# Performance work log

Measured on AMD Instinct MI355X. Metric: run time of the kernel, lower is better.

The kernel has to match this reference:

```python
import jax, jax.numpy as jnp
import numpy as np

B, S, D = 32, 4096, 512  # batch, src seq len, hidden (n_hidden_in == n_hidden_out)


def setup_inputs() -> dict:
    key = jax.random.key(0)
    k1, k2, k3, k4 = jax.random.split(key, 4)
    return {
        "hidden_targ": jax.random.normal(k1, (B, D), dtype=jnp.float32),
        "hidden_src": jax.random.normal(k2, (B, S, D), dtype=jnp.float32),
        "mask": jnp.ones((B, S), dtype=jnp.float32),
        "W": jax.random.normal(k3, (D, 2 * D), dtype=jnp.float32) * (2 * D) ** -0.5,
        "V": jax.random.uniform(k4, (D,), dtype=jnp.float32),
    }


def reference(hidden_targ, hidden_src, mask, W, V):
    # W @ cat(targ, src) == targ @ Wt^T + src @ Ws^T  (avoids materializing the
    # repeated/concatenated [b, s, 2d] tensor the torch code builds)
    d = hidden_targ.shape[-1]
    Wt, Ws = W[:, :d], W[:, d:]
    # [b, 1, h] + [b, s, h] -> tanh pre-activation
    pre = jnp.tanh(
        jnp.einsum("bd,hd->bh", hidden_targ, Wt)[:, None, :]
        + jnp.einsum("bsd,hd->bsh", hidden_src, Ws)
    )
    e = jnp.einsum("bsh,h->bs", pre, V)            # scores [b, s]
    att_weights = jax.nn.softmax(e, axis=1) * mask  # softmax then mask (as in source)
    ctx = jnp.einsum("bs,bsd->bd", att_weights, hidden_src)
    hidden_output = ctx + hidden_targ
    return att_weights, hidden_output
```

## Files before the change

### kernel.cpp

```cpp
#include <hip/hip_runtime.h>
#include <hip/hip_bf16.h>


typedef __attribute__((ext_vector_type(8))) short bf16x8;
typedef __attribute__((ext_vector_type(4))) float f32x4;

#define BM 128
#define BN 128
#define BKK 32
#define LDA 40

static __device__ __forceinline__ unsigned pack2(float a, float b) {
    unsigned ua = __float_as_uint(a), ub = __float_as_uint(b);
    unsigned ra = (ua + 0x7fffu + ((ua >> 16) & 1u)) >> 16;
    unsigned rb = (ub + 0x7fffu + ((ub >> 16) & 1u)) & 0xffff0000u;
    return ra | rb;
}

static __device__ __forceinline__ void async_load16(const void* g, void* l) {
    __builtin_amdgcn_global_load_lds(
        (const __attribute__((address_space(1))) void*)g,
        (__attribute__((address_space(3))) void*)l, 16, 0, 0);
}

static __device__ __forceinline__ float fast_tanh(float x) {
    float ex = exp2f(x * 2.8853900817779268f);
    return 1.0f - 2.0f / (ex + 1.0f);
}

__global__ void wconv_kernel(const float* __restrict__ W, short* __restrict__ wbf) {
    const int gid = blockIdx.x * 256 + threadIdx.x;
    const int tile = gid >> 9, p = gid & 511;
    const int hx = tile >> 4, ktile = tile & 15;
    const int r = p >> 2, up = p & 3;
    const int u = up ^ ((r >> 1) & 3);
    const float* s = W + (long)(hx * 128 + r) * 1024 + 512 + ktile * 32 + u * 8;
    float4 v0 = *(const float4*)(s);
    float4 v1 = *(const float4*)(s + 4);
    uint4 pk;
    pk.x = pack2(v0.x, v0.y); pk.y = pack2(v0.z, v0.w);
    pk.z = pack2(v1.x, v1.y); pk.w = pack2(v1.z, v1.w);
    ((uint4*)wbf)[gid] = pk;
}

__global__ void t_kernel(const float* __restrict__ targ,
                         const float* __restrict__ W,
                         float* __restrict__ t) {
    __shared__ float tg[512];
    const int b = blockIdx.x >> 2;
    const int hbase = (blockIdx.x & 3) * 128;
    const int tid = threadIdx.x;
    tg[tid]       = targ[b * 512 + tid];
    tg[tid + 256] = targ[b * 512 + tid + 256];
    __syncthreads();
    const int lane = tid & 63, wave = tid >> 6;
    for (int h = hbase + wave; h < hbase + 128; h += 4) {
        const float* wr = W + (long)h * 1024;
        float s = 0.f;
        #pragma unroll
        for (int i = 0; i < 2; i++) {
            const int d = lane * 4 + i * 256;
            float4 wv = *(const float4*)(wr + d);
            s += wv.x * tg[d] + wv.y * tg[d + 1] + wv.z * tg[d + 2] + wv.w * tg[d + 3];
        }
        s += __shfl_xor(s, 1);  s += __shfl_xor(s, 2);  s += __shfl_xor(s, 4);
        s += __shfl_xor(s, 8);  s += __shfl_xor(s, 16); s += __shfl_xor(s, 32);
        if (lane == 0) t[b * 512 + h] = s;
    }
}

__global__ __launch_bounds__(256, 2)
void gemm_e_kernel(const float* __restrict__ src,
                   const short* __restrict__ wbf,
                   const float* __restrict__ t,
                   const float* __restrict__ V,
                   float* __restrict__ e) {
    __shared__ __align__(16) short As[BM * LDA];
    __shared__ __align__(16) short Bs[BN * BKK];

    const int tid = threadIdx.x;
    const int L = blockIdx.x;
    const int mt = (L >> 5) * 8 + (L & 7);
    const int hx = (L >> 3) & 3;
    const long m0 = (long)mt * BM;
    const int b = (int)(m0 >> 12);

    const int lane = tid & 63;
    const int wave = tid >> 6;
    const int wm = wave & 1, wn = wave >> 1;
    const int lr = lane & 15, quad = lane >> 4;

    f32x4 acc[4][4];
    #pragma unroll
    for (int i = 0; i < 4; i++)
        #pragma unroll
        for (int j = 0; j < 4; j++)
            acc[i][j] = (f32x4){0.f, 0.f, 0.f, 0.f};

    const int arow = tid >> 1, ah = (tid & 1) * 16;

    for (int kt = 0; kt < 512; kt += BKK) {
        __syncthreads();
        const short* chunk = wbf + (long)(hx * 16 + (kt >> 5)) * 4096;
        async_load16(chunk + tid * 8, Bs + tid * 8);
        async_load16(chunk + 2048 + tid * 8, Bs + 2048 + tid * 8);
        const float* ap = src + (m0 + arow) * 512 + kt + ah;
        float4 v0 = *(const float4*)(ap);
        float4 v1 = *(const float4*)(ap + 4);
        float4 v2 = *(const float4*)(ap + 8);
        float4 v3 = *(const float4*)(ap + 12);
        uint4 pA, pB;
        pA.x = pack2(v0.x, v0.y); pA.y = pack2(v0.z, v0.w);
        pA.z = pack2(v1.x, v1.y); pA.w = pack2(v1.z, v1.w);
        pB.x = pack2(v2.x, v2.y); pB.y = pack2(v2.z, v2.w);
        pB.z = pack2(v3.x, v3.y); pB.w = pack2(v3.z, v3.w);
        *(uint4*)(As + arow * LDA + ah)     = pA;
        *(uint4*)(As + arow * LDA + ah + 8) = pB;
        __syncthreads();

        bf16x8 af[4], bfr[4];
        #pragma unroll
        for (int mi = 0; mi < 4; mi++)
            af[mi] = *(const bf16x8*)(As + (wm * 64 + mi * 16 + lr) * LDA + quad * 8);
        #pragma unroll
        for (int ni = 0; ni < 4; ni++) {
            const int row = wn * 64 + ni * 16 + lr;
            const int q = quad ^ ((row >> 1) & 3);
            bfr[ni] = *(const bf16x8*)(Bs + row * 32 + q * 8);
        }
        #pragma unroll
        for (int mi = 0; mi < 4; mi++)
            #pragma unroll
            for (int ni = 0; ni < 4; ni++)
                acc[mi][ni] = __builtin_amdgcn_mfma_f32_16x16x32_bf16(
                    af[mi], bfr[ni], acc[mi][ni], 0, 0, 0);
    }

    const float* trow = t + b * 512;
    float th[4], vv[4];
    #pragma unroll
    for (int ni = 0; ni < 4; ni++) {
        const int h = hx * 128 + wn * 64 + ni * 16 + lr;
        th[ni] = trow[h];
        vv[ni] = V[h];
    }
    #pragma unroll
    for (int mi = 0; mi < 4; mi++) {
        #pragma unroll
        for (int r = 0; r < 4; r++) {
            float es = 0.f;
            #pragma unroll
            for (int ni = 0; ni < 4; ni++) {
                float val = acc[mi][ni][r] + th[ni];
                es += fast_tanh(val) * vv[ni];
            }
            es += __shfl_xor(es, 1);
            es += __shfl_xor(es, 2);
            es += __shfl_xor(es, 4);
            es += __shfl_xor(es, 8);
            if (lr == 0) {
                const long m = m0 + wm * 64 + mi * 16 + quad * 4 + r;
                atomicAdd(&e[m], es);
            }
        }
    }
}

__global__ void stats_kernel(const float* __restrict__ e, float* __restrict__ stats) {
    const int b = blockIdx.x, tid = threadIdx.x;
    __shared__ float red[256];
    float mx = -1e30f;
    for (int s = tid; s < 4096; s += 256) mx = fmaxf(mx, e[b * 4096 + s]);
    red[tid] = mx; __syncthreads();
    for (int st = 128; st > 0; st >>= 1) {
        if (tid < st) red[tid] = fmaxf(red[tid], red[tid + st]);
        __syncthreads();
    }
    mx = red[0]; __syncthreads();
    float sm = 0.f;
    for (int s = tid; s < 4096; s += 256)
        sm += exp2f((e[b * 4096 + s] - mx) * 1.4426950408889634f);
    red[tid] = sm; __syncthreads();
    for (int st = 128; st > 0; st >>= 1) {
        if (tid < st) red[tid] += red[tid + st];
        __syncthreads();
    }
    if (tid == 0) { stats[b * 2] = mx; stats[b * 2 + 1] = red[0]; }
}

__global__ __launch_bounds__(256)
void ctx_kernel(const float* __restrict__ e, const float* __restrict__ stats,
                const float* __restrict__ mask, const float* __restrict__ src,
                float* __restrict__ att, float* __restrict__ outh) {
    const int b = blockIdx.y;
    const int s0 = blockIdx.x * 256;
    const int tid = threadIdx.x;
    __shared__ float ash[256];
    __shared__ float4 part[128];

    const float mx = stats[b * 2];
    const float inv = 1.0f / stats[b * 2 + 1];
    const int s = s0 + tid;
    float a = exp2f((e[b * 4096 + s] - mx) * 1.4426950408889634f) * inv
              * mask[b * 4096 + s];
    att[(long)b * 4096 + s] = a;
    ash[tid] = a;
    __syncthreads();

    const int half = tid >> 7, d4 = tid & 127;
    float4 acc = {0.f, 0.f, 0.f, 0.f};
    const float4* s4 = (const float4*)(src + ((long)b * 4096 + s0) * 512);
    #pragma unroll 4
    for (int i = half; i < 256; i += 2) {
        float4 v = s4[(long)i * 128 + d4];
        float w = ash[i];
        acc.x += w * v.x; acc.y += w * v.y; acc.z += w * v.z; acc.w += w * v.w;
    }
    if (half) part[d4] = acc;
    __syncthreads();
    if (!half) {
        float4 p = part[d4];
        acc.x += p.x; acc.y += p.y; acc.z += p.z; acc.w += p.w;
        float* o = outh + b * 512 + d4 * 4;
        atomicAdd(o + 0, acc.x); atomicAdd(o + 1, acc.y);
        atomicAdd(o + 2, acc.z); atomicAdd(o + 3, acc.w);
    }
}

extern "C" void kernel_launch(void* const* d_in, const int* in_sizes, int n_in,
                              void* d_out, int out_size, void* d_ws, size_t ws_size,
                              hipStream_t stream) {
    const float* targ = (const float*)d_in[0];
    const float* src  = (const float*)d_in[1];
    const float* mask = (const float*)d_in[2];
    const float* W    = (const float*)d_in[3];
    const float* V    = (const float*)d_in[4];

    float* att  = (float*)d_out;
    float* outh = (float*)d_out + 131072;

    float* e  = (float*)d_ws;
    float* t  = e + 131072;
    float* st = t + 16384;
    short* wbf = (short*)((char*)d_ws + 590080);

    hipMemsetAsync(e, 0, 131072 * sizeof(float), stream);
    hipMemcpyAsync(outh, targ, 16384 * sizeof(float), hipMemcpyDeviceToDevice, stream);

    wconv_kernel<<<128, 256, 0, stream>>>(W, wbf);
    t_kernel<<<128, 256, 0, stream>>>(targ, W, t);
    gemm_e_kernel<<<4096, 256, 0, stream>>>(src, wbf, t, V, e);
    stats_kernel<<<32, 256, 0, stream>>>(e, st);
    ctx_kernel<<<dim3(16, 32), 256, 0, stream>>>(e, st, mask, src, att, outh);
}
```

Before: 503.8 us.

## Pre-convert src to swizzled bf16 and replace atomics with partial-sum buffers

When the workspace is large enough, a new kernel converts the whole src tensor once into a swizzled bf16 tile layout. The GEMM then streams it straight into LDS with async loads, and the context reduction reads the bf16 copy instead of fp32. This targets two costs: each src tile being converted to bf16 separately in all four h-blocks that reuse it, and the fp32 re-read in the ctx pass. Atomic accumulation of scores and context is replaced by per-block partial buffers, which a stats kernel and a new final kernel reduce, so the memset and copy launches go away. The trade-offs are an extra full pass writing 128MB of bf16, lower precision in the context sum, and reliance on a large workspace, with an fp32 fallback path otherwise.

Measured after the change: 553.2 us. +9.8%, slower.

```diff
diff --git a/kernel.cpp b/kernel.cpp
--- a/kernel.cpp
+++ b/kernel.cpp
@@ -6,7 +6,6 @@
 typedef __attribute__((ext_vector_type(4))) float f32x4;
 
 #define BM 128
-#define BN 128
 #define BKK 32
 #define LDA 40
 
@@ -17,6 +16,10 @@
     return ra | rb;
 }
 
+static __device__ __forceinline__ float bf2f(short s) {
+    return __uint_as_float(((unsigned)(unsigned short)s) << 16);
+}
+
 static __device__ __forceinline__ void async_load16(const void* g, void* l) {
     __builtin_amdgcn_global_load_lds(
         (const __attribute__((address_space(1))) void*)g,
@@ -27,6 +30,15 @@
     float ex = exp2f(x * 2.8853900817779268f);
     return 1.0f - 2.0f / (ex + 1.0f);
 }
+
+#define WS_WBF     0L
+#define WS_EPART   524288L
+#define WS_E       2621440L
+#define WS_T       3145728L
+#define WS_STATS   3211264L
+#define WS_CTXP    3211520L
+#define WS_SRCBF   4260096L
+#define WS_NEED_A  (WS_SRCBF + 134217728L)
 
 __global__ void wconv_kernel(const float* __restrict__ W, short* __restrict__ wbf) {
     const int gid = blockIdx.x * 256 + threadIdx.x;
@@ -43,6 +55,22 @@
     ((uint4*)wbf)[gid] = pk;
 }
 
+__global__ void srcconv_kernel(const float* __restrict__ src, short* __restrict__ sbf) {
+    const long gid = (long)blockIdx.x * 256 + threadIdx.x;
+    const long tile = gid >> 9;
+    const int p = (int)(gid & 511);
+    const long mt = tile >> 4; const int kt = (int)(tile & 15);
+    const int r = p >> 2, up = p & 3;
+    const int u = up ^ ((r >> 1) & 3);
+    const float* s = src + (mt * 128 + r) * 512 + kt * 32 + u * 8;
+    float4 v0 = *(const float4*)(s);
+    float4 v1 = *(const float4*)(s + 4);
+    uint4 pk;
+    pk.x = pack2(v0.x, v0.y); pk.y = pack2(v0.z, v0.w);
+    pk.z = pack2(v1.x, v1.y); pk.w = pack2(v1.z, v1.w);
+    ((uint4*)sbf)[gid] = pk;
+}
+
 __global__ void t_kernel(const float* __restrict__ targ,
                          const float* __restrict__ W,
                          float* __restrict__ t) {
@@ -69,14 +97,106 @@
     }
 }
 
-__global__ __launch_bounds__(256, 2)
-void gemm_e_kernel(const float* __restrict__ src,
+__global__ __launch_bounds__(256, 4)
+void gemm_a_kernel(const short* __restrict__ sbf,
                    const short* __restrict__ wbf,
                    const float* __restrict__ t,
                    const float* __restrict__ V,
-                   float* __restrict__ e) {
+                   float* __restrict__ epart) {
+    __shared__ __align__(16) short As[4096];
+    __shared__ __align__(16) short Bs[4096];
+    __shared__ float er[2][128];
+
+    const int tid = threadIdx.x;
+    const int L = blockIdx.x;
+    const int mt = (L >> 5) * 8 + (L & 7);
+    const int hx = (L >> 3) & 3;
+    const long m0 = (long)mt * BM;
+    const int b = (int)(m0 >> 12);
+
+    const int lane = tid & 63;
+    const int wave = tid >> 6;
+    const int wm = wave & 1, wn = wave >> 1;
+    const int lr = lane & 15, quad = lane >> 4;
+
+    f32x4 acc[4][4];
+    #pragma unroll
+    for (int i = 0; i < 4; i++)
+        #pragma unroll
+        for (int j = 0; j < 4; j++)
+            acc[i][j] = (f32x4){0.f, 0.f, 0.f, 0.f};
+
+    const short* abase = sbf + (long)mt * 16 * 4096;
+    const short* bbase = wbf + (long)hx * 16 * 4096;
+
+    for (int kk = 0; kk < 16; kk++) {
+        __syncthreads();
+        const short* ag = abase + kk * 4096;
+        const short* bg = bbase + kk * 4096;
+        async_load16(ag + tid * 8, As + tid * 8);
+        async_load16(ag + 2048 + tid * 8, As + 2048 + tid * 8);
+        async_load16(bg + tid * 8, Bs + tid * 8);
+        async_load16(bg + 2048 + tid * 8, Bs + 2048 + tid * 8);
+        __syncthreads();
+
+        bf16x8 af[4], bfr[4];
+        #pragma unroll
+        for (int mi = 0; mi < 4; mi++) {
+            const int row = wm * 64 + mi * 16 + lr;
+            const int q = quad ^ ((row >> 1) & 3);
+            af[mi] = *(const bf16x8*)(As + row * 32 + q * 8);
+        }
+        #pragma unroll
+        for (int ni = 0; ni < 4; ni++) {
+            const int row = wn * 64 + ni * 16 + lr;
+            const int q = quad ^ ((row >> 1) & 3);
+            bfr[ni] = *(const bf16x8*)(Bs + row * 32 + q * 8);
+        }
+        #pragma unroll
+        for (int mi = 0; mi < 4; mi++)
+            #pragma unroll
+            for (int ni = 0; ni < 4; ni++)
+                acc[mi][ni] = __builtin_amdgcn_mfma_f32_16x16x32_bf16(
+                    af[mi], bfr[ni], acc[mi][ni], 0, 0, 0);
+    }
+
+    const float* trow = t + b * 512;
+    float th[4], vv[4];
+    #pragma unroll
+    for (int ni = 0; ni < 4; ni++) {
+        const int h = hx * 128 + wn * 64 + ni * 16 + lr;
+        th[ni] = trow[h];
+        vv[ni] = V[h];
+    }
+    #pragma unroll
+    for (int mi = 0; mi < 4; mi++) {
+        #pragma unroll
+        for (int r = 0; r < 4; r++) {
+            float es = 0.f;
+            #pragma unroll
+            for (int ni = 0; ni < 4; ni++)
+                es += fast_tanh(acc[mi][ni][r] + th[ni]) * vv[ni];
+            es += __shfl_xor(es, 1);
+            es += __shfl_xor(es, 2);
+            es += __shfl_xor(es, 4);
+            es += __shfl_xor(es, 8);
+            if (lr == 0) er[wn][wm * 64 + mi * 16 + quad * 4 + r] = es;
+        }
+    }
+    __syncthreads();
+    if (tid < 128)
+        epart[(long)hx * 131072 + m0 + tid] = er[0][tid] + er[1][tid];
+}
+
+__global__ __launch_bounds__(256, 2)
+void gemm_b_kernel(const float* __restrict__ src,
+                   const short* __restrict__ wbf,
+                   const float* __restrict__ t,
+                   const float* __restrict__ V,
+                   float* __restrict__ epart) {
     __shared__ __align__(16) short As[BM * LDA];
-    __shared__ __align__(16) short Bs[BN * BKK];
+    __shared__ __align__(16) short Bs[4096];
+    __shared__ float er[2][128];
 
     const int tid = threadIdx.x;
     const int L = blockIdx.x;
@@ -150,27 +270,34 @@
         for (int r = 0; r < 4; r++) {
             float es = 0.f;
             #pragma unroll
-            for (int ni = 0; ni < 4; ni++) {
-                float val = acc[mi][ni][r] + th[ni];
-                es += fast_tanh(val) * vv[ni];
-            }
+            for (int ni = 0; ni < 4; ni++)
+                es += fast_tanh(acc[mi][ni][r] + th[ni]) * vv[ni];
             es += __shfl_xor(es, 1);
             es += __shfl_xor(es, 2);
             es += __shfl_xor(es, 4);
             es += __shfl_xor(es, 8);
-            if (lr == 0) {
-                const long m = m0 + wm * 64 + mi * 16 + quad * 4 + r;
-                atomicAdd(&e[m], es);
-            }
-        }
-    }
-}
-
-__global__ void stats_kernel(const float* __restrict__ e, float* __restrict__ stats) {
+            if (lr == 0) er[wn][wm * 64 + mi * 16 + quad * 4 + r] = es;
+        }
+    }
+    __syncthreads();
+    if (tid < 128)
+        epart[(long)hx * 131072 + m0 + tid] = er[0][tid] + er[1][tid];
+}
+
+__global__ void stats_kernel(const float* __restrict__ epart,
+                             float* __restrict__ e, float* __restrict__ stats) {
     const int b = blockIdx.x, tid = threadIdx.x;
     __shared__ float red[256];
+    float ev[16];
     float mx = -1e30f;
-    for (int s = tid; s < 4096; s += 256) mx = fmaxf(mx, e[b * 4096 + s]);
+    #pragma unroll
+    for (int i = 0; i < 16; i++) {
+        const long m = (long)b * 4096 + tid + i * 256;
+        float v = epart[m] + epart[131072 + m] + epart[262144 + m] + epart[393216 + m];
+        e[m] = v;
+        ev[i] = v;
+        mx = fmaxf(mx, v);
+    }
     red[tid] = mx; __syncthreads();
     for (int st = 128; st > 0; st >>= 1) {
         if (tid < st) red[tid] = fmaxf(red[tid], red[tid + st]);
@@ -178,8 +305,9 @@
     }
     mx = red[0]; __syncthreads();
     float sm = 0.f;
-    for (int s = tid; s < 4096; s += 256)
-        sm += exp2f((e[b * 4096 + s] - mx) * 1.4426950408889634f);
+    #pragma unroll
+    for (int i = 0; i < 16; i++)
+        sm += exp2f((ev[i] - mx) * 1.4426950408889634f);
     red[tid] = sm; __syncthreads();
     for (int st = 128; st > 0; st >>= 1) {
         if (tid < st) red[tid] += red[tid + st];
@@ -189,9 +317,53 @@
 }
 
 __global__ __launch_bounds__(256)
-void ctx_kernel(const float* __restrict__ e, const float* __restrict__ stats,
-                const float* __restrict__ mask, const float* __restrict__ src,
-                float* __restrict__ att, float* __restrict__ outh) {
+void ctx_bf_kernel(const float* __restrict__ e, const float* __restrict__ stats,
+                   const float* __restrict__ mask, const short* __restrict__ sbf,
+                   float* __restrict__ att, float* __restrict__ ctxpart) {
+    const int b = blockIdx.y;
+    const int s0 = blockIdx.x * 256;
+    const int tid = threadIdx.x;
+    __shared__ float ash[256];
+    __shared__ float part[4][512];
+
+    const float mx = stats[b * 2];
+    const float inv = 1.0f / stats[b * 2 + 1];
+    const int s = s0 + tid;
+    float a = exp2f((e[b * 4096 + s] - mx) * 1.4426950408889634f) * inv
+              * mask[b * 4096 + s];
+    att[(long)b * 4096 + s] = a;
+    ash[tid] = a;
+    __syncthreads();
+
+    const int phase = tid >> 6, uu = tid & 63;
+    const int kt = uu >> 2, u = uu & 3;
+    const long mt0 = ((long)b * 4096 + s0) >> 7;
+    float acc[8];
+    #pragma unroll
+    for (int j = 0; j < 8; j++) acc[j] = 0.f;
+
+    for (int i = phase; i < 256; i += 4) {
+        const long mt = mt0 + (i >> 7);
+        const int r = i & 127;
+        const short* p = sbf + (mt * 16 + kt) * 4096 + r * 32 + ((u ^ ((r >> 1) & 3))) * 8;
+        bf16x8 v = *(const bf16x8*)p;
+        const float w = ash[i];
+        #pragma unroll
+        for (int j = 0; j < 8; j++) acc[j] += w * bf2f(v[j]);
+    }
+    #pragma unroll
+    for (int j = 0; j < 8; j++) part[phase][uu * 8 + j] = acc[j];
+    __syncthreads();
+    for (int d = tid; d < 512; d += 256) {
+        float sv = part[0][d] + part[1][d] + part[2][d] + part[3][d];
+        ctxpart[((long)blockIdx.x * 32 + b) * 512 + d] = sv;
+    }
+}
+
+__global__ __launch_bounds__(256)
+void ctx_f32_kernel(const float* __restrict__ e, const float* __restrict__ stats,
+                    const float* __restrict__ mask, const float* __restrict__ src,
+                    float* __restrict__ att, float* __restrict__ ctxpart) {
     const int b = blockIdx.y;
     const int s0 = blockIdx.x * 256;
     const int tid = threadIdx.x;
@@ -221,10 +393,18 @@
     if (!half) {
         float4 p = part[d4];
         acc.x += p.x; acc.y += p.y; acc.z += p.z; acc.w += p.w;
-        float* o = outh + b * 512 + d4 * 4;
-        atomicAdd(o + 0, acc.x); atomicAdd(o + 1, acc.y);
-        atomicAdd(o + 2, acc.z); atomicAdd(o + 3, acc.w);
-    }
+        *(float4*)(ctxpart + ((long)blockIdx.x * 32 + b) * 512 + d4 * 4) = acc;
+    }
+}
+
+__global__ void final_kernel(const float* __restrict__ targ,
+                             const float* __restrict__ ctxpart,
+                             float* __restrict__ outh) {
+    const int g = blockIdx.x * 256 + threadIdx.x;
+    float sv = targ[g];
+    #pragma unroll
+    for (int x = 0; x < 16; x++) sv += ctxpart[(long)x * 16384 + g];
+    outh[g] = sv;
 }
 
 extern "C" void kernel_launch(void* const* d_in, const int* in_sizes, int n_in,
@@ -239,17 +419,28 @@
     float* att  = (float*)d_out;
     float* outh = (float*)d_out + 131072;
 
-    float* e  = (float*)d_ws;
-    float* t  = e + 131072;
-    float* st = t + 16384;
-    short* wbf = (short*)((char*)d_ws + 590080);
-
-    hipMemsetAsync(e, 0, 131072 * sizeof(float), stream);
-    hipMemcpyAsync(outh, targ, 16384 * sizeof(float), hipMemcpyDeviceToDevice, stream);
-
+    char* ws = (char*)d_ws;
+    short* wbf    = (short*)(ws + WS_WBF);
+    float* epart  = (float*)(ws + WS_EPART);
+    float* e      = (float*)(ws + WS_E);
+    float* t      = (float*)(ws + WS_T);
+    float* st     = (float*)(ws + WS_STATS);
+    float* ctxp   = (float*)(ws + WS_CTXP);
+    short* sbf    = (short*)(ws + WS_SRCBF);
+
+    const bool planA = ws_size >= (size_t)WS_NEED_A;
+
+    if (planA) srcconv_kernel<<<32768, 256, 0, stream>>>(src, sbf);
     wconv_kernel<<<128, 256, 0, stream>>>(W, wbf);
     t_kernel<<<128, 256, 0, stream>>>(targ, W, t);
-    gemm_e_kernel<<<4096, 256, 0, stream>>>(src, wbf, t, V, e);
-    stats_kernel<<<32, 256, 0, stream>>>(e, st);
-    ctx_kernel<<<dim3(16, 32), 256, 0, stream>>>(e, st, mask, src, att, outh);
-}
+    if (planA)
+        gemm_a_kernel<<<4096, 256, 0, stream>>>(sbf, wbf, t, V, epart);
+    else
+        gemm_b_kernel<<<4096, 256, 0, stream>>>(src, wbf, t, V, epart);
+    stats_kernel<<<32, 256, 0, stream>>>(epart, e, st);
+    if (planA)
+        ctx_bf_kernel<<<dim3(16, 32), 256, 0, stream>>>(e, st, mask, sbf, att, ctxp);
+    else
+        ctx_f32_kernel<<<dim3(16, 32), 256, 0, stream>>>(e, st, mask, src, att, ctxp);
+    final_kernel<<<64, 256, 0, stream>>>(targ, ctxp, outh);
+}
```

## Replace atomic accumulations with deterministic partial buffers and final reduction kernels

Applied to the files above, without the earlier changes.

The GEMM kernel now reduces scores across its two wn-waves in shared memory and writes one partial per hx slice to a buffer instead of issuing global atomicAdds. The stats kernel sums the four partials, writes e, and keeps the values in registers for the exp pass instead of reading them again. The context kernel writes per-block partials that a new final kernel sums together with targ. This removes the memset, the D2D copy and the atomic contention, and also switches the bf16 conversion to the HIP intrinsic, at the cost of one extra launch and some extra partial-buffer traffic.

New measurement: 494.9 us. About the same (-1.8%).

```diff
diff --git a/kernel.cpp b/kernel.cpp
--- a/kernel.cpp
+++ b/kernel.cpp
@@ -6,15 +6,13 @@
 typedef __attribute__((ext_vector_type(4))) float f32x4;
 
 #define BM 128
-#define BN 128
 #define BKK 32
 #define LDA 40
 
-static __device__ __forceinline__ unsigned pack2(float a, float b) {
-    unsigned ua = __float_as_uint(a), ub = __float_as_uint(b);
-    unsigned ra = (ua + 0x7fffu + ((ua >> 16) & 1u)) >> 16;
-    unsigned rb = (ub + 0x7fffu + ((ub >> 16) & 1u)) & 0xffff0000u;
-    return ra | rb;
+static __device__ __forceinline__ unsigned cvt2(float a, float b) {
+    union { __hip_bfloat162 h; unsigned u; } v;
+    v.h = __float22bfloat162_rn(make_float2(a, b));
+    return v.u;
 }
 
 static __device__ __forceinline__ void async_load16(const void* g, void* l) {
@@ -27,6 +25,13 @@
     float ex = exp2f(x * 2.8853900817779268f);
     return 1.0f - 2.0f / (ex + 1.0f);
 }
+
+#define WS_WBF     0L
+#define WS_EPART   524288L
+#define WS_E       2621440L
+#define WS_T       3145728L
+#define WS_STATS   3211264L
+#define WS_CTXP    3211520L
 
 __global__ void wconv_kernel(const float* __restrict__ W, short* __restrict__ wbf) {
     const int gid = blockIdx.x * 256 + threadIdx.x;
@@ -38,8 +43,8 @@
     float4 v0 = *(const float4*)(s);
     float4 v1 = *(const float4*)(s + 4);
     uint4 pk;
-    pk.x = pack2(v0.x, v0.y); pk.y = pack2(v0.z, v0.w);
-    pk.z = pack2(v1.x, v1.y); pk.w = pack2(v1.z, v1.w);
+    pk.x = cvt2(v0.x, v0.y); pk.y = cvt2(v0.z, v0.w);
+    pk.z = cvt2(v1.x, v1.y); pk.w = cvt2(v1.z, v1.w);
     ((uint4*)wbf)[gid] = pk;
 }
 
@@ -70,13 +75,14 @@
 }
 
 __global__ __launch_bounds__(256, 2)
-void gemm_e_kernel(const float* __restrict__ src,
-                   const short* __restrict__ wbf,
-                   const float* __restrict__ t,
-                   const float* __restrict__ V,
-                   float* __restrict__ e) {
+void gemm_kernel(const float* __restrict__ src,
+                 const short* __restrict__ wbf,
+                 const float* __restrict__ t,
+                 const float* __restrict__ V,
+                 float* __restrict__ epart) {
     __shared__ __align__(16) short As[BM * LDA];
-    __shared__ __align__(16) short Bs[BN * BKK];
+    __shared__ __align__(16) short Bs[4096];
+    __shared__ float er[2][128];
 
     const int tid = threadIdx.x;
     const int L = blockIdx.x;
@@ -110,10 +116,10 @@
         float4 v2 = *(const float4*)(ap + 8);
         float4 v3 = *(const float4*)(ap + 12);
         uint4 pA, pB;
-        pA.x = pack2(v0.x, v0.y); pA.y = pack2(v0.z, v0.w);
-        pA.z = pack2(v1.x, v1.y); pA.w = pack2(v1.z, v1.w);
-        pB.x = pack2(v2.x, v2.y); pB.y = pack2(v2.z, v2.w);
-        pB.z = pack2(v3.x, v3.y); pB.w = pack2(v3.z, v3.w);
+        pA.x = cvt2(v0.x, v0.y); pA.y = cvt2(v0.z, v0.w);
+        pA.z = cvt2(v1.x, v1.y); pA.w = cvt2(v1.z, v1.w);
+        pB.x = cvt2(v2.x, v2.y); pB.y = cvt2(v2.z, v2.w);
+        pB.z = cvt2(v3.x, v3.y); pB.w = cvt2(v3.z, v3.w);
         *(uint4*)(As + arow * LDA + ah)     = pA;
         *(uint4*)(As + arow * LDA + ah + 8) = pB;
         __syncthreads();
@@ -150,27 +156,34 @@
         for (int r = 0; r < 4; r++) {
             float es = 0.f;
             #pragma unroll
-            for (int ni = 0; ni < 4; ni++) {
-                float val = acc[mi][ni][r] + th[ni];
-                es += fast_tanh(val) * vv[ni];
-            }
+            for (int ni = 0; ni < 4; ni++)
+                es += fast_tanh(acc[mi][ni][r] + th[ni]) * vv[ni];
             es += __shfl_xor(es, 1);
             es += __shfl_xor(es, 2);
             es += __shfl_xor(es, 4);
             es += __shfl_xor(es, 8);
-            if (lr == 0) {
-                const long m = m0 + wm * 64 + mi * 16 + quad * 4 + r;
-                atomicAdd(&e[m], es);
-            }
+            if (lr == 0) er[wn][wm * 64 + mi * 16 + quad * 4 + r] = es;
         }
     }
-}
-
-__global__ void stats_kernel(const float* __restrict__ e, float* __restrict__ stats) {
+    __syncthreads();
+    if (tid < 128)
+        epart[(long)hx * 131072 + m0 + tid] = er[0][tid] + er[1][tid];
+}
+
+__global__ void stats_kernel(const float* __restrict__ epart,
+                             float* __restrict__ e, float* __restrict__ stats) {
     const int b = blockIdx.x, tid = threadIdx.x;
     __shared__ float red[256];
+    float ev[16];
     float mx = -1e30f;
-    for (int s = tid; s < 4096; s += 256) mx = fmaxf(mx, e[b * 4096 + s]);
+    #pragma unroll
+    for (int i = 0; i < 16; i++) {
+        const long m = (long)b * 4096 + tid + i * 256;
+        float v = epart[m] + epart[131072 + m] + epart[262144 + m] + epart[393216 + m];
+        e[m] = v;
+        ev[i] = v;
+        mx = fmaxf(mx, v);
+    }
     red[tid] = mx; __syncthreads();
     for (int st = 128; st > 0; st >>= 1) {
         if (tid < st) red[tid] = fmaxf(red[tid], red[tid + st]);
@@ -178,8 +191,9 @@
     }
     mx = red[0]; __syncthreads();
     float sm = 0.f;
-    for (int s = tid; s < 4096; s += 256)
-        sm += exp2f((e[b * 4096 + s] - mx) * 1.4426950408889634f);
+    #pragma unroll
+    for (int i = 0; i < 16; i++)
+        sm += exp2f((ev[i] - mx) * 1.4426950408889634f);
     red[tid] = sm; __syncthreads();
     for (int st = 128; st > 0; st >>= 1) {
         if (tid < st) red[tid] += red[tid + st];
@@ -191,7 +205,7 @@
 __global__ __launch_bounds__(256)
 void ctx_kernel(const float* __restrict__ e, const float* __restrict__ stats,
                 const float* __restrict__ mask, const float* __restrict__ src,
-                float* __restrict__ att, float* __restrict__ outh) {
+                float* __restrict__ att, float* __restrict__ ctxpart) {
     const int b = blockIdx.y;
     const int s0 = blockIdx.x * 256;
     const int tid = threadIdx.x;
@@ -221,10 +235,18 @@
     if (!half) {
         float4 p = part[d4];
         acc.x += p.x; acc.y += p.y; acc.z += p.z; acc.w += p.w;
-        float* o = outh + b * 512 + d4 * 4;
-        atomicAdd(o + 0, acc.x); atomicAdd(o + 1, acc.y);
-        atomicAdd(o + 2, acc.z); atomicAdd(o + 3, acc.w);
-    }
+        *(float4*)(ctxpart + ((long)blockIdx.x * 32 + b) * 512 + d4 * 4) = acc;
+    }
+}
+
+__global__ void final_kernel(const float* __restrict__ targ,
+                             const float* __restrict__ ctxpart,
+                             float* __restrict__ outh) {
+    const int g = blockIdx.x * 256 + threadIdx.x;
+    float sv = targ[g];
+    #pragma unroll
+    for (int x = 0; x < 16; x++) sv += ctxpart[(long)x * 16384 + g];
+    outh[g] = sv;
 }
 
 extern "C" void kernel_launch(void* const* d_in, const int* in_sizes, int n_in,
@@ -239,17 +261,18 @@
     float* att  = (float*)d_out;
     float* outh = (float*)d_out + 131072;
 
-    float* e  = (float*)d_ws;
-    float* t  = e + 131072;
-    float* st = t + 16384;
-    short* wbf = (short*)((char*)d_ws + 590080);
-
-    hipMemsetAsync(e, 0, 131072 * sizeof(float), stream);
-    hipMemcpyAsync(outh, targ, 16384 * sizeof(float), hipMemcpyDeviceToDevice, stream);
+    char* ws = (char*)d_ws;
+    short* wbf    = (short*)(ws + WS_WBF);
+    float* epart  = (float*)(ws + WS_EPART);
+    float* e      = (float*)(ws + WS_E);
+    float* t      = (float*)(ws + WS_T);
+    float* st     = (float*)(ws + WS_STATS);
+    float* ctxp   = (float*)(ws + WS_CTXP);
 
     wconv_kernel<<<128, 256, 0, stream>>>(W, wbf);
     t_kernel<<<128, 256, 0, stream>>>(targ, W, t);
-    gemm_e_kernel<<<4096, 256, 0, stream>>>(src, wbf, t, V, e);
-    stats_kernel<<<32, 256, 0, stream>>>(e, st);
-    ctx_kernel<<<dim3(16, 32), 256, 0, stream>>>(e, st, mask, src, att, outh);
-}
+    gemm_kernel<<<4096, 256, 0, stream>>>(src, wbf, t, V, epart);
+    stats_kernel<<<32, 256, 0, stream>>>(epart, e, st);
+    ctx_kernel<<<dim3(16, 32), 256, 0, stream>>>(e, st, mask, src, att, ctxp);
+    final_kernel<<<64, 256, 0, stream>>>(targ, ctxp, outh);
+}
```
